# Optimization experiments

Measured on AMD Instinct MI355X. Metric: run time of the kernel, lower is better.

The kernel has to match this reference:

```python
import jax, jax.numpy as jnp
import numpy as np

B, N, IN_C, OUT_C = 32, 1024, 64, 128
ALPHA = 0.2  # LeakyReLU negative slope
NEG_INF = -1e16


def setup_inputs() -> dict:
    key = jax.random.key(0)
    k1, k2, k3, k4, k5 = jax.random.split(key, 5)
    inputs = jax.random.normal(k1, (B, N, IN_C), dtype=jnp.float32)
    # dense 0/1 adjacency mask
    graph = jax.random.randint(k2, (N, N), 0, 2).astype(jnp.float32)
    # torch nn.Linear weight layout: [out_c, in_c]
    W = jax.random.normal(k3, (OUT_C, IN_C), dtype=jnp.float32)
    b = jax.random.normal(k4, (OUT_C,), dtype=jnp.float32)
    a = jax.random.normal(k5, (2 * OUT_C, 1), dtype=jnp.float32)
    return {"inputs": inputs, "graph": graph, "W": W, "b": b, "a": a}


def reference(inputs, graph, W, b, a):
    # h = W(inputs): [B, N, D]
    h = jnp.einsum('bnt,dt->bnd', inputs, W)
    # cat([h_i, h_j]) @ a  ==  h_i @ a1 + h_j @ a2  (decomposed, no [B,N,N,2D] tensor)
    a1 = a[:OUT_C, 0]   # [D]
    a2 = a[OUT_C:, 0]   # [D]
    s1 = jnp.einsum('bnd,d->bn', h, a1)  # score contribution of node i
    s2 = jnp.einsum('bnd,d->bn', h, a2)  # score contribution of node j
    e = s1[:, :, None] + s2[:, None, :]  # [B, N, N]
    e = jnp.where(e > 0, e, ALPHA * e)   # LeakyReLU
    e = e * graph                        # zero out non-edges
    # torch masked_fill_(eq(outputs, 0), -1e16)
    e = jnp.where(e == 0.0, NEG_INF, e)
    attention = jax.nn.softmax(e, axis=2)  # [B, N, N]
    out = jnp.einsum('bij,bjd->bid', attention, h) + b  # [B, N, D]
    return out
```

## Files before the change

kernel.cpp:

```cpp
#include <hip/hip_runtime.h>
#include <hip/hip_bf16.h>

#define ALPHA 0.2f

typedef unsigned short ushort_t;
typedef unsigned short ushort8 __attribute__((ext_vector_type(8)));
typedef float f32x4 __attribute__((ext_vector_type(4)));
typedef __bf16 bf16x8 __attribute__((ext_vector_type(8)));

__device__ __forceinline__ ushort_t f2bf(float f) {
  unsigned u = __float_as_uint(f);
  u += 0x7fffu + ((u >> 16) & 1u);
  return (ushort_t)(u >> 16);
}
__device__ __forceinline__ float bf2f(ushort_t b) {
  return __uint_as_float((unsigned)b << 16);
}

__global__ __launch_bounds__(128) void gat_h_kernel(
    const float* __restrict__ inp, const float* __restrict__ W,
    const float* __restrict__ avec, ushort_t* __restrict__ hT,
    float* __restrict__ s1, float* __restrict__ s2)
{
  const int b  = blockIdx.x >> 5;
  const int n0 = (blockIdx.x & 31) << 5;
  const int t  = threadIdx.x;

  __shared__ float    x_lds[32 * 64];
  __shared__ ushort_t h_tile[128][40];
  __shared__ float    s1p[2][32];
  __shared__ float    s2p[2][32];

  float wreg[64];
  {
    const float4* wrow = (const float4*)(W + t * 64);
#pragma unroll
    for (int k = 0; k < 16; ++k) {
      float4 v = wrow[k];
      wreg[4*k+0] = v.x; wreg[4*k+1] = v.y; wreg[4*k+2] = v.z; wreg[4*k+3] = v.w;
    }
  }
  const float a1 = avec[t];
  const float a2 = avec[128 + t];

  {
    const float4* xsrc = (const float4*)(inp + ((size_t)b * 1024 + n0) * 64);
    float4* xdst = (float4*)x_lds;
#pragma unroll
    for (int k = 0; k < 4; ++k) xdst[k * 128 + t] = xsrc[k * 128 + t];
  }
  __syncthreads();

  const int wv = t >> 6, ln = t & 63;
  for (int r = 0; r < 32; ++r) {
    const float4* xr = (const float4*)(x_lds + r * 64);
    float ax = 0.f, ay = 0.f, az = 0.f, aw = 0.f;
#pragma unroll
    for (int k = 0; k < 16; ++k) {
      float4 xv = xr[k];
      ax = fmaf(wreg[4*k+0], xv.x, ax);
      ay = fmaf(wreg[4*k+1], xv.y, ay);
      az = fmaf(wreg[4*k+2], xv.z, az);
      aw = fmaf(wreg[4*k+3], xv.w, aw);
    }
    const float h = (ax + ay) + (az + aw);
    h_tile[t][r] = f2bf(h);
    float v1 = h * a1, v2 = h * a2;
#pragma unroll
    for (int m = 32; m >= 1; m >>= 1) {
      v1 += __shfl_xor(v1, m);
      v2 += __shfl_xor(v2, m);
    }
    if (ln == 0) { s1p[wv][r] = v1; s2p[wv][r] = v2; }
  }
  __syncthreads();

  if (t < 32) {
    s1[(size_t)b * 1024 + n0 + t] = s1p[0][t] + s1p[1][t];
    s2[(size_t)b * 1024 + n0 + t] = s2p[0][t] + s2p[1][t];
  }

#pragma unroll
  for (int it = 0; it < 4; ++it) {
    const int d  = it * 32 + (t >> 2);
    const int ch = (t & 3) * 8;
    ushort8 v = *(const ushort8*)&h_tile[d][ch];
    *(ushort8*)(hT + ((size_t)b * 128 + d) * 1024 + n0 + ch) = v;
  }
}

__global__ __launch_bounds__(256) void gat_attn_kernel(
    const float* __restrict__ graph, const ushort_t* __restrict__ hT,
    const float* __restrict__ s1g, const float* __restrict__ s2g,
    const float* __restrict__ bias, float* __restrict__ out)
{
  const int ic = blockIdx.x;
  const int b  = blockIdx.y;
  const int i0 = ic << 5;
  const int t  = threadIdx.x;
  const int w  = t >> 6;
  const int l  = t & 63;

  __shared__ float    s2_lds[1024];
  __shared__ ushort_t p_lds[32][72];
  __shared__ ushort_t ht_lds[128][72];
  __shared__ float    red_part[32][8];
  __shared__ float    red_row[32];

  {
    const float4* src = (const float4*)(s2g + (size_t)b * 1024);
    ((float4*)s2_lds)[t] = src[t];
  }
  const int irow = t >> 3;
  const int jsl  = (t & 7) * 8;
  const float s1v = s1g[(size_t)b * 1024 + i0 + irow];
  const float* grow = graph + (size_t)(i0 + irow) * 1024 + jsl;
  const ushort_t* htb = hT + (size_t)b * 128 * 1024;
  __syncthreads();

  float mx_local = -1e30f;
  for (int jt = 0; jt < 16; ++jt) {
    const int j0 = jt * 64;
    float4 g0 = *(const float4*)(grow + j0);
    float4 g1 = *(const float4*)(grow + j0 + 4);
    float4 sA = *(const float4*)(s2_lds + j0 + jsl);
    float4 sB = *(const float4*)(s2_lds + j0 + jsl + 4);
    if (g0.x != 0.f) mx_local = fmaxf(mx_local, sA.x);
    if (g0.y != 0.f) mx_local = fmaxf(mx_local, sA.y);
    if (g0.z != 0.f) mx_local = fmaxf(mx_local, sA.z);
    if (g0.w != 0.f) mx_local = fmaxf(mx_local, sA.w);
    if (g1.x != 0.f) mx_local = fmaxf(mx_local, sB.x);
    if (g1.y != 0.f) mx_local = fmaxf(mx_local, sB.y);
    if (g1.z != 0.f) mx_local = fmaxf(mx_local, sB.z);
    if (g1.w != 0.f) mx_local = fmaxf(mx_local, sB.w);
  }
  red_part[irow][t & 7] = mx_local;
  __syncthreads();
  if (t < 32) {
    float m = red_part[t][0];
#pragma unroll
    for (int k = 1; k < 8; ++k) m = fmaxf(m, red_part[t][k]);
    red_row[t] = m;
  }
  __syncthreads();
  const float tm = s1v + red_row[irow];
  const float Mi = tm > 0.f ? tm : ALPHA * tm;
  __syncthreads();

  float den_local = 0.f;
  f32x4 c[2][2];
#pragma unroll
  for (int is = 0; is < 2; ++is)
#pragma unroll
    for (int ds = 0; ds < 2; ++ds)
      c[is][ds] = f32x4{0.f, 0.f, 0.f, 0.f};

  for (int jt = 0; jt < 16; ++jt) {
    const int j0 = jt * 64;
    ushort8 hv[4];
#pragma unroll
    for (int k = 0; k < 4; ++k) {
      const int c2 = t + k * 256;
      const int d  = c2 >> 3;
      const int jc = (c2 & 7) * 8;
      hv[k] = *(const ushort8*)(htb + (size_t)d * 1024 + j0 + jc);
    }
    float4 g0 = *(const float4*)(grow + j0);
    float4 g1 = *(const float4*)(grow + j0 + 4);
    float4 sA = *(const float4*)(s2_lds + j0 + jsl);
    float4 sB = *(const float4*)(s2_lds + j0 + jsl + 4);
    float gg[8] = {g0.x, g0.y, g0.z, g0.w, g1.x, g1.y, g1.z, g1.w};
    float ss[8] = {sA.x, sA.y, sA.z, sA.w, sB.x, sB.y, sB.z, sB.w};
    ushort8 pb;
#pragma unroll
    for (int e = 0; e < 8; ++e) {
      float te = s1v + ss[e];
      float v  = te > 0.f ? te : ALPHA * te;
      float p  = (gg[e] != 0.f && v != 0.f) ? __expf(v - Mi) : 0.f;
      pb[e] = f2bf(p);
      den_local += bf2f(pb[e]);
    }
    *(ushort8*)&p_lds[irow][jsl] = pb;
#pragma unroll
    for (int k = 0; k < 4; ++k) {
      const int c2 = t + k * 256;
      const int d  = c2 >> 3;
      const int jc = (c2 & 7) * 8;
      *(ushort8*)&ht_lds[d][jc] = hv[k];
    }
    __syncthreads();
#pragma unroll
    for (int kk = 0; kk < 2; ++kk) {
      const int kcol = kk * 32 + (l >> 4) * 8;
      bf16x8 av[2];
#pragma unroll
      for (int is = 0; is < 2; ++is)
        av[is] = __builtin_bit_cast(
            bf16x8, *(const ushort8*)&p_lds[is * 16 + (l & 15)][kcol]);
#pragma unroll
      for (int ds = 0; ds < 2; ++ds) {
        bf16x8 bv = __builtin_bit_cast(
            bf16x8,
            *(const ushort8*)&ht_lds[w * 32 + ds * 16 + (l & 15)][kcol]);
#pragma unroll
        for (int is = 0; is < 2; ++is)
          c[is][ds] = __builtin_amdgcn_mfma_f32_16x16x32_bf16(
              av[is], bv, c[is][ds], 0, 0, 0);
      }
    }
    __syncthreads();
  }

  red_part[irow][t & 7] = den_local;
  __syncthreads();
  if (t < 32) {
    float s = red_part[t][0];
#pragma unroll
    for (int k = 1; k < 8; ++k) s += red_part[t][k];
    red_row[t] = s;
  }
  __syncthreads();

#pragma unroll
  for (int ds = 0; ds < 2; ++ds) {
    const int col = w * 32 + ds * 16 + (l & 15);
    const float bc = bias[col];
#pragma unroll
    for (int is = 0; is < 2; ++is) {
#pragma unroll
      for (int r = 0; r < 4; ++r) {
        const int row = is * 16 + (l >> 4) * 4 + r;
        const float dr = red_row[row];
        const float val = dr > 0.f ? c[is][ds][r] / dr + bc : bc;
        out[((size_t)b * 1024 + i0 + row) * 128 + col] = val;
      }
    }
  }
}

extern "C" void kernel_launch(void* const* d_in, const int* in_sizes, int n_in,
                              void* d_out, int out_size, void* d_ws, size_t ws_size,
                              hipStream_t stream) {
  (void)in_sizes; (void)n_in; (void)out_size; (void)ws_size;
  const float* inp   = (const float*)d_in[0];
  const float* graph = (const float*)d_in[1];
  const float* W     = (const float*)d_in[2];
  const float* bias  = (const float*)d_in[3];
  const float* avec  = (const float*)d_in[4];
  float* out = (float*)d_out;

  ushort_t* hT = (ushort_t*)d_ws;
  float* s1 = (float*)((char*)d_ws + (size_t)32 * 128 * 1024 * 2);
  float* s2 = s1 + 32 * 1024;

  gat_h_kernel<<<1024, 128, 0, stream>>>(inp, W, avec, hT, s1, s2);
  gat_attn_kernel<<<dim3(32, 32), 256, 0, stream>>>(graph, hT, s1, s2, bias, out);
}
```

Baseline: 67.09 us.

## Bit-pack adjacency mask, precompute W^T a for scores, widen h kernel tiles

```diff
diff --git a/kernel.cpp b/kernel.cpp
--- a/kernel.cpp
+++ b/kernel.cpp
@@ -4,6 +4,7 @@
 #define ALPHA 0.2f
 
 typedef unsigned short ushort_t;
+typedef unsigned int   uint_t;
 typedef unsigned short ushort8 __attribute__((ext_vector_type(8)));
 typedef float f32x4 __attribute__((ext_vector_type(4)));
 typedef __bf16 bf16x8 __attribute__((ext_vector_type(8)));
@@ -17,80 +18,123 @@
   return __uint_as_float((unsigned)b << 16);
 }
 
-__global__ __launch_bounds__(128) void gat_h_kernel(
+__global__ __launch_bounds__(128) void gat_u_kernel(
+    const float* __restrict__ W, const float* __restrict__ avec,
+    float* __restrict__ u)
+{
+  const int t  = threadIdx.x;
+  const int k  = t & 63;
+  const int ao = (t >> 6) * 128;
+  float a0 = 0.f, a1 = 0.f, a2 = 0.f, a3 = 0.f;
+  for (int d = 0; d < 128; d += 4) {
+    a0 = fmaf(avec[ao + d + 0], W[(d + 0) * 64 + k], a0);
+    a1 = fmaf(avec[ao + d + 1], W[(d + 1) * 64 + k], a1);
+    a2 = fmaf(avec[ao + d + 2], W[(d + 2) * 64 + k], a2);
+    a3 = fmaf(avec[ao + d + 3], W[(d + 3) * 64 + k], a3);
+  }
+  u[t] = (a0 + a1) + (a2 + a3);
+}
+
+__global__ __launch_bounds__(256) void gat_pack_kernel(
+    const float* __restrict__ graph, uint_t* __restrict__ gmask)
+{
+  const int row = blockIdx.x, t = threadIdx.x;
+  __shared__ uint_t nibs[256];
+  float4 g = ((const float4*)(graph + (size_t)row * 1024))[t];
+  uint_t nib = (g.x != 0.f ? 1u : 0u) | (g.y != 0.f ? 2u : 0u) |
+               (g.z != 0.f ? 4u : 0u) | (g.w != 0.f ? 8u : 0u);
+  nibs[t] = nib;
+  __syncthreads();
+  if (t < 32) {
+    uint_t w = 0;
+#pragma unroll
+    for (int k = 0; k < 8; ++k) w |= nibs[t * 8 + k] << (4 * k);
+    gmask[(size_t)row * 32 + t] = w;
+  }
+}
+
+__global__ __launch_bounds__(256) void gat_h_kernel(
     const float* __restrict__ inp, const float* __restrict__ W,
-    const float* __restrict__ avec, ushort_t* __restrict__ hT,
+    const float* __restrict__ uvec, ushort_t* __restrict__ hT,
     float* __restrict__ s1, float* __restrict__ s2)
 {
-  const int b  = blockIdx.x >> 5;
-  const int n0 = (blockIdx.x & 31) << 5;
+  const int b  = blockIdx.x >> 4;
+  const int n0 = (blockIdx.x & 15) << 6;
   const int t  = threadIdx.x;
-
-  __shared__ float    x_lds[32 * 64];
-  __shared__ ushort_t h_tile[128][40];
-  __shared__ float    s1p[2][32];
-  __shared__ float    s2p[2][32];
+  const int d  = t & 127;
+  const int nh = t >> 7;
+
+  __shared__ float    x_lds[64][68];
+  __shared__ float    u_lds[128];
+  __shared__ ushort_t h_tile[128][72];
 
   float wreg[64];
   {
-    const float4* wrow = (const float4*)(W + t * 64);
+    const float4* wrow = (const float4*)(W + d * 64);
 #pragma unroll
     for (int k = 0; k < 16; ++k) {
       float4 v = wrow[k];
       wreg[4*k+0] = v.x; wreg[4*k+1] = v.y; wreg[4*k+2] = v.z; wreg[4*k+3] = v.w;
     }
   }
-  const float a1 = avec[t];
-  const float a2 = avec[128 + t];
+  if (t < 128) u_lds[t] = uvec[t];
 
   {
     const float4* xsrc = (const float4*)(inp + ((size_t)b * 1024 + n0) * 64);
-    float4* xdst = (float4*)x_lds;
-#pragma unroll
-    for (int k = 0; k < 4; ++k) xdst[k * 128 + t] = xsrc[k * 128 + t];
-  }
-  __syncthreads();
-
-  const int wv = t >> 6, ln = t & 63;
+#pragma unroll
+    for (int k = 0; k < 4; ++k) {
+      const int g = k * 256 + t;
+      const int n = g >> 4, c = g & 15;
+      *(float4*)&x_lds[n][c * 4] = xsrc[g];
+    }
+  }
+  __syncthreads();
+
   for (int r = 0; r < 32; ++r) {
-    const float4* xr = (const float4*)(x_lds + r * 64);
+    const int n = nh * 32 + r;
+    const float* xr = &x_lds[n][0];
     float ax = 0.f, ay = 0.f, az = 0.f, aw = 0.f;
 #pragma unroll
     for (int k = 0; k < 16; ++k) {
-      float4 xv = xr[k];
+      float4 xv = *(const float4*)&xr[4 * k];
       ax = fmaf(wreg[4*k+0], xv.x, ax);
       ay = fmaf(wreg[4*k+1], xv.y, ay);
       az = fmaf(wreg[4*k+2], xv.z, az);
       aw = fmaf(wreg[4*k+3], xv.w, aw);
     }
-    const float h = (ax + ay) + (az + aw);
-    h_tile[t][r] = f2bf(h);
-    float v1 = h * a1, v2 = h * a2;
-#pragma unroll
-    for (int m = 32; m >= 1; m >>= 1) {
-      v1 += __shfl_xor(v1, m);
-      v2 += __shfl_xor(v2, m);
-    }
-    if (ln == 0) { s1p[wv][r] = v1; s2p[wv][r] = v2; }
-  }
-  __syncthreads();
-
-  if (t < 32) {
-    s1[(size_t)b * 1024 + n0 + t] = s1p[0][t] + s1p[1][t];
-    s2[(size_t)b * 1024 + n0 + t] = s2p[0][t] + s2p[1][t];
-  }
+    h_tile[d][n] = f2bf((ax + ay) + (az + aw));
+  }
+
+  if (t < 128) {
+    const int n = t & 63, which = t >> 6;
+    const float* xr = &x_lds[n][0];
+    const float* uu = &u_lds[which * 64];
+    float a0 = 0.f, a1 = 0.f, a2 = 0.f, a3 = 0.f;
+#pragma unroll
+    for (int k = 0; k < 16; ++k) {
+      float4 xv = *(const float4*)&xr[4 * k];
+      a0 = fmaf(xv.x, uu[4*k+0], a0);
+      a1 = fmaf(xv.y, uu[4*k+1], a1);
+      a2 = fmaf(xv.z, uu[4*k+2], a2);
+      a3 = fmaf(xv.w, uu[4*k+3], a3);
+    }
+    const float sv = (a0 + a1) + (a2 + a3);
+    if (which == 0) s1[(size_t)b * 1024 + n0 + n] = sv;
+    else            s2[(size_t)b * 1024 + n0 + n] = sv;
+  }
+  __syncthreads();
 
 #pragma unroll
   for (int it = 0; it < 4; ++it) {
-    const int d  = it * 32 + (t >> 2);
-    const int ch = (t & 3) * 8;
-    ushort8 v = *(const ushort8*)&h_tile[d][ch];
-    *(ushort8*)(hT + ((size_t)b * 128 + d) * 1024 + n0 + ch) = v;
+    const int d2 = it * 32 + (t >> 3);
+    const int ch = (t & 7) * 8;
+    ushort8 v = *(const ushort8*)&h_tile[d2][ch];
+    *(ushort8*)(hT + ((size_t)b * 128 + d2) * 1024 + n0 + ch) = v;
   }
 }
 
 __global__ __launch_bounds__(256) void gat_attn_kernel(
-    const float* __restrict__ graph, const ushort_t* __restrict__ hT,
+    const uint_t* __restrict__ gmask, const ushort_t* __restrict__ hT,
     const float* __restrict__ s1g, const float* __restrict__ s2g,
     const float* __restrict__ bias, float* __restrict__ out)
 {
@@ -102,6 +146,7 @@
   const int l  = t & 63;
 
   __shared__ float    s2_lds[1024];
+  __shared__ uint_t   mask_lds[32][33];
   __shared__ ushort_t p_lds[32][72];
   __shared__ ushort_t ht_lds[128][72];
   __shared__ float    red_part[32][8];
@@ -111,28 +156,34 @@
     const float4* src = (const float4*)(s2g + (size_t)b * 1024);
     ((float4*)s2_lds)[t] = src[t];
   }
+  {
+    const uint4 mv = ((const uint4*)(gmask + (size_t)(i0 + (t >> 3)) * 32))[t & 7];
+    const int mr = t >> 3, mc = (t & 7) * 4;
+    mask_lds[mr][mc + 0] = mv.x; mask_lds[mr][mc + 1] = mv.y;
+    mask_lds[mr][mc + 2] = mv.z; mask_lds[mr][mc + 3] = mv.w;
+  }
   const int irow = t >> 3;
   const int jsl  = (t & 7) * 8;
+  const int bo   = (t & 3) * 8;
+  const int widx = (t >> 2) & 1;
   const float s1v = s1g[(size_t)b * 1024 + i0 + irow];
-  const float* grow = graph + (size_t)(i0 + irow) * 1024 + jsl;
   const ushort_t* htb = hT + (size_t)b * 128 * 1024;
   __syncthreads();
 
   float mx_local = -1e30f;
   for (int jt = 0; jt < 16; ++jt) {
     const int j0 = jt * 64;
-    float4 g0 = *(const float4*)(grow + j0);
-    float4 g1 = *(const float4*)(grow + j0 + 4);
+    const uint_t word = mask_lds[irow][jt * 2 + widx];
     float4 sA = *(const float4*)(s2_lds + j0 + jsl);
     float4 sB = *(const float4*)(s2_lds + j0 + jsl + 4);
-    if (g0.x != 0.f) mx_local = fmaxf(mx_local, sA.x);
-    if (g0.y != 0.f) mx_local = fmaxf(mx_local, sA.y);
-    if (g0.z != 0.f) mx_local = fmaxf(mx_local, sA.z);
-    if (g0.w != 0.f) mx_local = fmaxf(mx_local, sA.w);
-    if (g1.x != 0.f) mx_local = fmaxf(mx_local, sB.x);
-    if (g1.y != 0.f) mx_local = fmaxf(mx_local, sB.y);
-    if (g1.z != 0.f) mx_local = fmaxf(mx_local, sB.z);
-    if (g1.w != 0.f) mx_local = fmaxf(mx_local, sB.w);
+    if ((word >> (bo + 0)) & 1u) mx_local = fmaxf(mx_local, sA.x);
+    if ((word >> (bo + 1)) & 1u) mx_local = fmaxf(mx_local, sA.y);
+    if ((word >> (bo + 2)) & 1u) mx_local = fmaxf(mx_local, sA.z);
+    if ((word >> (bo + 3)) & 1u) mx_local = fmaxf(mx_local, sA.w);
+    if ((word >> (bo + 4)) & 1u) mx_local = fmaxf(mx_local, sB.x);
+    if ((word >> (bo + 5)) & 1u) mx_local = fmaxf(mx_local, sB.y);
+    if ((word >> (bo + 6)) & 1u) mx_local = fmaxf(mx_local, sB.z);
+    if ((word >> (bo + 7)) & 1u) mx_local = fmaxf(mx_local, sB.w);
   }
   red_part[irow][t & 7] = mx_local;
   __syncthreads();
@@ -161,22 +212,20 @@
 #pragma unroll
     for (int k = 0; k < 4; ++k) {
       const int c2 = t + k * 256;
-      const int d  = c2 >> 3;
+      const int dd = c2 >> 3;
       const int jc = (c2 & 7) * 8;
-      hv[k] = *(const ushort8*)(htb + (size_t)d * 1024 + j0 + jc);
-    }
-    float4 g0 = *(const float4*)(grow + j0);
-    float4 g1 = *(const float4*)(grow + j0 + 4);
+      hv[k] = *(const ushort8*)(htb + (size_t)dd * 1024 + j0 + jc);
+    }
+    const uint_t word = mask_lds[irow][jt * 2 + widx];
     float4 sA = *(const float4*)(s2_lds + j0 + jsl);
     float4 sB = *(const float4*)(s2_lds + j0 + jsl + 4);
-    float gg[8] = {g0.x, g0.y, g0.z, g0.w, g1.x, g1.y, g1.z, g1.w};
     float ss[8] = {sA.x, sA.y, sA.z, sA.w, sB.x, sB.y, sB.z, sB.w};
     ushort8 pb;
 #pragma unroll
     for (int e = 0; e < 8; ++e) {
       float te = s1v + ss[e];
       float v  = te > 0.f ? te : ALPHA * te;
-      float p  = (gg[e] != 0.f && v != 0.f) ? __expf(v - Mi) : 0.f;
+      float p = (((word >> (bo + e)) & 1u) && v != 0.f) ? __expf(v - Mi) : 0.f;
       pb[e] = f2bf(p);
       den_local += bf2f(pb[e]);
     }
@@ -184,9 +233,9 @@
 #pragma unroll
     for (int k = 0; k < 4; ++k) {
       const int c2 = t + k * 256;
-      const int d  = c2 >> 3;
+      const int dd = c2 >> 3;
       const int jc = (c2 & 7) * 8;
-      *(ushort8*)&ht_lds[d][jc] = hv[k];
+      *(ushort8*)&ht_lds[dd][jc] = hv[k];
     }
     __syncthreads();
 #pragma unroll
@@ -249,10 +298,15 @@
   const float* avec  = (const float*)d_in[4];
   float* out = (float*)d_out;
 
-  ushort_t* hT = (ushort_t*)d_ws;
-  float* s1 = (float*)((char*)d_ws + (size_t)32 * 128 * 1024 * 2);
-  float* s2 = s1 + 32 * 1024;
-
-  gat_h_kernel<<<1024, 128, 0, stream>>>(inp, W, avec, hT, s1, s2);
-  gat_attn_kernel<<<dim3(32, 32), 256, 0, stream>>>(graph, hT, s1, s2, bias, out);
-}
+  char* ws = (char*)d_ws;
+  ushort_t* hT = (ushort_t*)ws;
+  float* s1    = (float*)(ws + (size_t)8 * 1024 * 1024);
+  float* s2    = s1 + 32 * 1024;
+  float* u     = s2 + 32 * 1024;
+  uint_t* gm   = (uint_t*)(ws + (size_t)8 * 1024 * 1024 + 512 * 1024);
+
+  gat_pack_kernel<<<1024, 256, 0, stream>>>(graph, gm);
+  gat_u_kernel<<<1, 128, 0, stream>>>(W, avec, u);
+  gat_h_kernel<<<512, 256, 0, stream>>>(inp, W, u, hT, s1, s2);
+  gat_attn_kernel<<<dim3(32, 32), 256, 0, stream>>>(gm, hT, s1, s2, bias, out);
+}
```

Result: no change. 68.37 us (+1.9%).
